# Performance work log

Hardware: AMD Instinct MI355X
Metric: run time of the kernel (lower is better)

The kernel has to match this reference:

```python
import jax, jax.numpy as jnp
import numpy as np

B, T, C, H = 4, 4096, 1024, 64

def setup_inputs() -> dict:
    key = jax.random.key(0)
    kx, kk, kq, kv = jax.random.split(key, 4)
    x = jax.random.normal(kx, (B, T, C), dtype=jnp.float32)
    # causal lower-triangular mask; masked_fill where mask == 0
    mask = jnp.tril(jnp.ones((T, T), dtype=jnp.int32))
    s = 1.0 / np.sqrt(C)
    Wk = jax.random.normal(kk, (H, C), dtype=jnp.float32) * s
    Wq = jax.random.normal(kq, (H, C), dtype=jnp.float32) * s
    Wv = jax.random.normal(kv, (H, C), dtype=jnp.float32) * s
    return {"x": x, "mask": mask, "Wk": Wk, "Wq": Wq, "Wv": Wv}

def reference(x, mask, Wk, Wq, Wv):
    # single-head attention; dropout is identity in eval mode
    scale = Wk.shape[0] ** -0.5  # head_size ** -0.5
    k = jnp.einsum('btc,hc->bth', x, Wk)  # [B,T,H]
    q = jnp.einsum('btc,hc->bth', x, Wq)
    v = jnp.einsum('btc,hc->bth', x, Wv)
    att = jnp.einsum('bqh,bkh->bqk', q, k) * scale  # [B,T,T]
    att = jnp.where(mask == 0, -jnp.inf, att)
    att = jax.nn.softmax(att, axis=-1)
    out = jnp.einsum('bqk,bkh->bqh', att, v)  # [B,T,H]
    return out
```

## Files before the change

### kernel.cpp

```cpp
#include <hip/hip_runtime.h>
#include <hip/hip_bf16.h>

#define BT 16384
#define CDIM 1024
#define HD 64
#define TT 4096

typedef __bf16 bf16x8 __attribute__((ext_vector_type(8)));
typedef __bf16 bf16x4 __attribute__((ext_vector_type(4)));
typedef float f32x4 __attribute__((ext_vector_type(4)));

__device__ __forceinline__ f32x4 mfma16(bf16x8 a, bf16x8 b, f32x4 c){
  return __builtin_amdgcn_mfma_f32_16x16x32_bf16(a, b, c, 0, 0, 0);
}

__global__ __launch_bounds__(256) void wconv_k(const float* __restrict__ Wk,
    const float* __restrict__ Wq, const float* __restrict__ Wv,
    __bf16* __restrict__ Wbf){
  int idx = blockIdx.x*256 + threadIdx.x;
  int e0 = idx*4;
  int n = e0 >> 10;
  int c = e0 & 1023;
  const float* src; float s;
  if (n < 64)      { src = Wk + (size_t)n*CDIM;       s = 1.0f;   }
  else if (n < 128){ src = Wq + (size_t)(n-64)*CDIM;  s = 0.125f; }
  else             { src = Wv + (size_t)(n-128)*CDIM; s = 1.0f;   }
  float4 v = *reinterpret_cast<const float4*>(src + c);
  __bf16* dst = Wbf + e0;
  dst[0]=(__bf16)(v.x*s); dst[1]=(__bf16)(v.y*s);
  dst[2]=(__bf16)(v.z*s); dst[3]=(__bf16)(v.w*s);
}

__global__ __launch_bounds__(512) void proj_k(const float* __restrict__ x,
    const __bf16* __restrict__ Wbf, __bf16* __restrict__ kb,
    __bf16* __restrict__ qb, __bf16* __restrict__ vTb){
  __shared__ __bf16 Wt[192][72];
  __shared__ __bf16 Xt[64][72];

  const int tid  = threadIdx.x;
  const int lane = tid & 63;
  const int w    = tid >> 6;
  const int wr   = w >> 2;
  const int wn   = w & 3;
  const int l15  = lane & 15, g = lane >> 4;
  const long row0 = (long)blockIdx.x*64;

  f32x4 acc[2][3];
  #pragma unroll
  for (int a=0;a<2;a++)
    #pragma unroll
    for (int b=0;b<3;b++) acc[a][b] = (f32x4)(0.0f);

  for (int kk=0; kk<16; ++kk){
    const int kk0 = kk*64;
    __syncthreads();
    #pragma unroll
    for (int i=0;i<3;i++){
      const int c  = tid + 512*i;
      const int rw = c >> 3, c8 = (c & 7)*8;
      bf16x8 wv = *reinterpret_cast<const bf16x8*>(Wbf + (size_t)rw*CDIM + kk0 + c8);
      *reinterpret_cast<bf16x8*>(&Wt[rw][c8]) = wv;
    }
    {
      const int rw = tid >> 3, c8 = (tid & 7)*8;
      const float* src = x + (row0 + rw)*CDIM + kk0 + c8;
      float4 lo = *reinterpret_cast<const float4*>(src);
      float4 hi = *reinterpret_cast<const float4*>(src + 4);
      bf16x8 xv;
      xv[0]=(__bf16)lo.x; xv[1]=(__bf16)lo.y; xv[2]=(__bf16)lo.z; xv[3]=(__bf16)lo.w;
      xv[4]=(__bf16)hi.x; xv[5]=(__bf16)hi.y; xv[6]=(__bf16)hi.z; xv[7]=(__bf16)hi.w;
      *reinterpret_cast<bf16x8*>(&Xt[rw][c8]) = xv;
    }
    __syncthreads();

    bf16x8 a0[2], a1[2], b0[3], b1[3];
    #pragma unroll
    for (int rf=0;rf<2;rf++){
      a0[rf] = *reinterpret_cast<const bf16x8*>(&Xt[wr*32 + rf*16 + l15][g*8]);
      a1[rf] = *reinterpret_cast<const bf16x8*>(&Xt[wr*32 + rf*16 + l15][g*8 + 32]);
    }
    #pragma unroll
    for (int nf=0;nf<3;nf++){
      b0[nf] = *reinterpret_cast<const bf16x8*>(&Wt[wn*48 + nf*16 + l15][g*8]);
      b1[nf] = *reinterpret_cast<const bf16x8*>(&Wt[wn*48 + nf*16 + l15][g*8 + 32]);
    }
    #pragma unroll
    for (int rf=0;rf<2;rf++)
      #pragma unroll
      for (int nf=0;nf<3;nf++)
        acc[rf][nf] = mfma16(a1[rf], b1[nf], mfma16(a0[rf], b0[nf], acc[rf][nf]));
  }

  const long bidx = row0 >> 12;
  #pragma unroll
  for (int nf=0;nf<3;nf++){
    const int n0  = wn*48 + nf*16 + l15;
    const int mat = n0 >> 6;
    const int h   = n0 & 63;
    #pragma unroll
    for (int rf=0;rf<2;rf++){
      const long rbase = row0 + wr*32 + rf*16 + g*4;
      if (mat == 0){
        #pragma unroll
        for (int r=0;r<4;r++) kb[(rbase+r)*HD + h] = (__bf16)acc[rf][nf][r];
      } else if (mat == 1){
        #pragma unroll
        for (int r=0;r<4;r++) qb[(rbase+r)*HD + h] = (__bf16)acc[rf][nf][r];
      } else {
        bf16x4 t4;
        #pragma unroll
        for (int r=0;r<4;r++) t4[r] = (__bf16)acc[rf][nf][r];
        *reinterpret_cast<bf16x4*>(vTb + (bidx*64 + h)*TT + (rbase & 4095)) = t4;
      }
    }
  }
}

template<int NS>
__global__ __launch_bounds__(256) void attn_part_k(const __bf16* __restrict__ kbg,
    const __bf16* __restrict__ qbg, const __bf16* __restrict__ vT,
    __bf16* __restrict__ po, float* __restrict__ pl){
  __shared__ __bf16 Klds[64][68];
  __shared__ __bf16 Vlds[64][68];
  __shared__ __bf16 Plds[4][16][68];

  const int tid  = threadIdx.x;
  const int lane = tid & 63;
  const int w    = tid >> 6;
  const int l15  = lane & 15, g = lane >> 4;

  const int bi  = blockIdx.x;
  const int b   = bi / (64*NS);
  const int rem = bi % (64*NS);
  const int qt  = 63 - rem / NS;
  const int s   = rem % NS;

  const int ntiles = qt + 1;
  const int lo = ( s      * ntiles) / NS;
  const int hi = ((s + 1) * ntiles) / NS;
  const int pidx = (b*64 + qt)*NS + s;

  if (lo == hi){
    if (l15 == 0){
      #pragma unroll
      for (int r=0;r<4;r++) pl[pidx*64 + w*16 + g*4 + r] = 0.0f;
    }
    return;
  }

  const long qbase = (long)b*TT + (long)qt*64;

  bf16x8 qf0, qf1;
  {
    const __bf16* src = qbg + (qbase + w*16 + l15)*HD + g*8;
    qf0 = *reinterpret_cast<const bf16x8*>(src);
    qf1 = *reinterpret_cast<const bf16x8*>(src + 32);
  }

  f32x4 o[4];
  #pragma unroll
  for (int ch=0; ch<4; ++ch) o[ch] = (f32x4)(0.0f);
  float lp[4] = {0.f, 0.f, 0.f, 0.f};

  const __bf16* vbase = vT + (size_t)b*64*TT;

  for (int kv=lo; kv<hi; ++kv){
    const long kvbase = (long)b*TT + (long)kv*64;
    const int  kvt    = kv*64;

    __syncthreads();
    {
      const int key = tid >> 2;
      const int d0  = (tid & 3) * 16;
      const __bf16* ks = kbg + (kvbase + key)*HD + d0;
      *reinterpret_cast<bf16x8*>(&Klds[key][d0])   = *reinterpret_cast<const bf16x8*>(ks);
      *reinterpret_cast<bf16x8*>(&Klds[key][d0+8]) = *reinterpret_cast<const bf16x8*>(ks+8);
      const int h    = tid >> 2;
      const int key0 = (tid & 3) * 16;
      const __bf16* vs = vbase + (size_t)h*TT + kvt + key0;
      *reinterpret_cast<bf16x8*>(&Vlds[h][key0])   = *reinterpret_cast<const bf16x8*>(vs);
      *reinterpret_cast<bf16x8*>(&Vlds[h][key0+8]) = *reinterpret_cast<const bf16x8*>(vs+8);
    }
    __syncthreads();

    f32x4 sv[4];
    #pragma unroll
    for (int c=0;c<4;c++){
      bf16x8 kb0 = *reinterpret_cast<const bf16x8*>(&Klds[c*16 + l15][g*8]);
      bf16x8 kb1 = *reinterpret_cast<const bf16x8*>(&Klds[c*16 + l15][g*8 + 32]);
      sv[c] = mfma16(qf0, kb0, (f32x4)(-16.0f));
      sv[c] = mfma16(qf1, kb1, sv[c]);
    }

    if (kv == qt){
      #pragma unroll
      for (int c=0;c<4;c++){
        const int key = c*16 + l15;
        #pragma unroll
        for (int r=0;r<4;r++){
          const int qr = w*16 + g*4 + r;
          if (key > qr) sv[c][r] = -1e30f;
        }
      }
    }

    #pragma unroll
    for (int c=0;c<4;c++){
      #pragma unroll
      for (int r=0;r<4;r++) sv[c][r] = __expf(sv[c][r]);
    }
    #pragma unroll
    for (int r=0;r<4;r++)
      lp[r] += (sv[0][r] + sv[1][r]) + (sv[2][r] + sv[3][r]);

    #pragma unroll
    for (int c=0;c<4;c++){
      #pragma unroll
      for (int r=0;r<4;r++) Plds[w][g*4+r][c*16 + l15] = (__bf16)sv[c][r];
    }
    asm volatile("s_waitcnt lgkmcnt(0)" ::: "memory");
    __builtin_amdgcn_sched_barrier(0);
    bf16x8 pa0 = *reinterpret_cast<const bf16x8*>(&Plds[w][l15][g*8]);
    bf16x8 pa1 = *reinterpret_cast<const bf16x8*>(&Plds[w][l15][g*8 + 32]);

    #pragma unroll
    for (int ch=0; ch<4; ++ch){
      bf16x8 vb0 = *reinterpret_cast<const bf16x8*>(&Vlds[ch*16 + l15][g*8]);
      bf16x8 vb1 = *reinterpret_cast<const bf16x8*>(&Vlds[ch*16 + l15][g*8 + 32]);
      o[ch] = mfma16(pa0, vb0, o[ch]);
      o[ch] = mfma16(pa1, vb1, o[ch]);
    }
  }

  float lr[4];
  #pragma unroll
  for (int r=0;r<4;r++){
    float v = lp[r];
    v += __shfl_xor(v, 1);
    v += __shfl_xor(v, 2);
    v += __shfl_xor(v, 4);
    v += __shfl_xor(v, 8);
    lr[r] = v;
  }
  float rl[4];
  #pragma unroll
  for (int r=0;r<4;r++) rl[r] = (lr[r] > 0.0f) ? 1.0f/lr[r] : 0.0f;

  __bf16* podst = po + (size_t)pidx*4096;
  #pragma unroll
  for (int ch=0; ch<4; ++ch){
    #pragma unroll
    for (int r=0;r<4;r++)
      podst[(w*16 + g*4 + r)*64 + ch*16 + l15] = (__bf16)(o[ch][r] * rl[r]);
  }
  if (l15 == 0){
    #pragma unroll
    for (int r=0;r<4;r++) pl[pidx*64 + w*16 + g*4 + r] = lr[r];
  }
}

template<int NS>
__global__ __launch_bounds__(256) void comb_k(const __bf16* __restrict__ po,
    const float* __restrict__ pl, float* __restrict__ out){
  const int idx   = blockIdx.x*256 + threadIdx.x;
  const int qrow  = idx >> 6;
  const int dim   = idx & 63;
  const int qtg   = qrow >> 6;
  const int rowin = qrow & 63;

  float num = 0.0f, den = 0.0f;
  #pragma unroll
  for (int s=0;s<NS;s++){
    const float l = pl[(qtg*NS + s)*64 + rowin];
    den += l;
    num += l * (float)po[(size_t)(qtg*NS + s)*4096 + rowin*64 + dim];
  }
  out[idx] = num / den;
}

extern "C" void kernel_launch(void* const* d_in, const int* in_sizes, int n_in,
                              void* d_out, int out_size, void* d_ws, size_t ws_size,
                              hipStream_t stream) {
  const float* x  = (const float*)d_in[0];
  const float* Wk = (const float*)d_in[2];
  const float* Wq = (const float*)d_in[3];
  const float* Wv = (const float*)d_in[4];
  float* out = (float*)d_out;

  char* ws = (char*)d_ws;
  __bf16* Wbf = (__bf16*)ws;
  __bf16* kb  = (__bf16*)(ws + 393216);
  __bf16* qb  = (__bf16*)(ws + 2490368);
  __bf16* vTb = (__bf16*)(ws + 4587520);
  __bf16* po  = (__bf16*)(ws + 6684672);

  wconv_k<<<192, 256, 0, stream>>>(Wk, Wq, Wv, Wbf);
  proj_k <<<256, 512, 0, stream>>>(x, Wbf, kb, qb, vTb);

  const size_t need8 = 6684672ull + (size_t)2048*4096*2 + (size_t)2048*64*4;
  if (ws_size >= need8){
    float* pl = (float*)(ws + 6684672 + (size_t)2048*4096*2);
    attn_part_k<8><<<2048, 256, 0, stream>>>(kb, qb, vTb, po, pl);
    comb_k<8>    <<<4096, 256, 0, stream>>>(po, pl, out);
  } else {
    float* pl = (float*)(ws + 6684672 + (size_t)1024*4096*2);
    attn_part_k<4><<<1024, 256, 0, stream>>>(kb, qb, vTb, po, pl);
    comb_k<4>    <<<4096, 256, 0, stream>>>(po, pl, out);
  }
}
```

Before: 65.26 us.

## Register-prefetch next tiles in projection and attention loops

Both the projection GEMM loop and the attention KV loop now load the next tile's global data into registers right after the LDS barrier, then write it to shared memory at the start of the next iteration. The aim is to hide global-memory latency behind the MFMA compute of the current tile. This adds register pressure, which could lower occupancy.

```diff
diff --git a/kernel.cpp b/kernel.cpp
--- a/kernel.cpp
+++ b/kernel.cpp
@@ -45,33 +45,50 @@
   const int l15  = lane & 15, g = lane >> 4;
   const long row0 = (long)blockIdx.x*64;
 
+  const int wrw[3] = { (tid)>>3, (tid+512)>>3, (tid+1024)>>3 };
+  const int wc8[3] = { (tid&7)*8, (tid&7)*8, (tid&7)*8 };
+  const int xrw = tid >> 3, xc8 = (tid & 7)*8;
+
   f32x4 acc[2][3];
   #pragma unroll
   for (int a=0;a<2;a++)
     #pragma unroll
     for (int b=0;b<3;b++) acc[a][b] = (f32x4)(0.0f);
 
+  bf16x8 wreg[3];
+  float4 xlo, xhi;
+
+  #pragma unroll
+  for (int i=0;i<3;i++)
+    wreg[i] = *reinterpret_cast<const bf16x8*>(Wbf + (size_t)wrw[i]*CDIM + wc8[i]);
+  {
+    const float* src = x + (row0 + xrw)*CDIM + xc8;
+    xlo = *reinterpret_cast<const float4*>(src);
+    xhi = *reinterpret_cast<const float4*>(src + 4);
+  }
+
   for (int kk=0; kk<16; ++kk){
-    const int kk0 = kk*64;
     __syncthreads();
     #pragma unroll
-    for (int i=0;i<3;i++){
-      const int c  = tid + 512*i;
-      const int rw = c >> 3, c8 = (c & 7)*8;
-      bf16x8 wv = *reinterpret_cast<const bf16x8*>(Wbf + (size_t)rw*CDIM + kk0 + c8);
-      *reinterpret_cast<bf16x8*>(&Wt[rw][c8]) = wv;
-    }
+    for (int i=0;i<3;i++)
+      *reinterpret_cast<bf16x8*>(&Wt[wrw[i]][wc8[i]]) = wreg[i];
     {
-      const int rw = tid >> 3, c8 = (tid & 7)*8;
-      const float* src = x + (row0 + rw)*CDIM + kk0 + c8;
-      float4 lo = *reinterpret_cast<const float4*>(src);
-      float4 hi = *reinterpret_cast<const float4*>(src + 4);
       bf16x8 xv;
-      xv[0]=(__bf16)lo.x; xv[1]=(__bf16)lo.y; xv[2]=(__bf16)lo.z; xv[3]=(__bf16)lo.w;
-      xv[4]=(__bf16)hi.x; xv[5]=(__bf16)hi.y; xv[6]=(__bf16)hi.z; xv[7]=(__bf16)hi.w;
-      *reinterpret_cast<bf16x8*>(&Xt[rw][c8]) = xv;
+      xv[0]=(__bf16)xlo.x; xv[1]=(__bf16)xlo.y; xv[2]=(__bf16)xlo.z; xv[3]=(__bf16)xlo.w;
+      xv[4]=(__bf16)xhi.x; xv[5]=(__bf16)xhi.y; xv[6]=(__bf16)xhi.z; xv[7]=(__bf16)xhi.w;
+      *reinterpret_cast<bf16x8*>(&Xt[xrw][xc8]) = xv;
     }
     __syncthreads();
+
+    if (kk < 15){
+      const int nk0 = (kk+1)*64;
+      #pragma unroll
+      for (int i=0;i<3;i++)
+        wreg[i] = *reinterpret_cast<const bf16x8*>(Wbf + (size_t)wrw[i]*CDIM + nk0 + wc8[i]);
+      const float* src = x + (row0 + xrw)*CDIM + nk0 + xc8;
+      xlo = *reinterpret_cast<const float4*>(src);
+      xhi = *reinterpret_cast<const float4*>(src + 4);
+    }
 
     bf16x8 a0[2], a1[2], b0[3], b1[3];
     #pragma unroll
@@ -164,24 +181,37 @@
 
   const __bf16* vbase = vT + (size_t)b*64*TT;
 
+  const int skey = tid >> 2;
+  const int sd0  = (tid & 3) * 16;
+  bf16x8 kr0, kr1, vr0, vr1;
+
+  {
+    const long kvbase = (long)b*TT + (long)lo*64;
+    const __bf16* ks = kbg + (kvbase + skey)*HD + sd0;
+    kr0 = *reinterpret_cast<const bf16x8*>(ks);
+    kr1 = *reinterpret_cast<const bf16x8*>(ks+8);
+    const __bf16* vs = vbase + (size_t)skey*TT + lo*64 + sd0;
+    vr0 = *reinterpret_cast<const bf16x8*>(vs);
+    vr1 = *reinterpret_cast<const bf16x8*>(vs+8);
+  }
+
   for (int kv=lo; kv<hi; ++kv){
-    const long kvbase = (long)b*TT + (long)kv*64;
-    const int  kvt    = kv*64;
-
     __syncthreads();
-    {
-      const int key = tid >> 2;
-      const int d0  = (tid & 3) * 16;
-      const __bf16* ks = kbg + (kvbase + key)*HD + d0;
-      *reinterpret_cast<bf16x8*>(&Klds[key][d0])   = *reinterpret_cast<const bf16x8*>(ks);
-      *reinterpret_cast<bf16x8*>(&Klds[key][d0+8]) = *reinterpret_cast<const bf16x8*>(ks+8);
-      const int h    = tid >> 2;
-      const int key0 = (tid & 3) * 16;
-      const __bf16* vs = vbase + (size_t)h*TT + kvt + key0;
-      *reinterpret_cast<bf16x8*>(&Vlds[h][key0])   = *reinterpret_cast<const bf16x8*>(vs);
-      *reinterpret_cast<bf16x8*>(&Vlds[h][key0+8]) = *reinterpret_cast<const bf16x8*>(vs+8);
-    }
+    *reinterpret_cast<bf16x8*>(&Klds[skey][sd0])   = kr0;
+    *reinterpret_cast<bf16x8*>(&Klds[skey][sd0+8]) = kr1;
+    *reinterpret_cast<bf16x8*>(&Vlds[skey][sd0])   = vr0;
+    *reinterpret_cast<bf16x8*>(&Vlds[skey][sd0+8]) = vr1;
     __syncthreads();
+
+    if (kv+1 < hi){
+      const long nbase = (long)b*TT + (long)(kv+1)*64;
+      const __bf16* ks = kbg + (nbase + skey)*HD + sd0;
+      kr0 = *reinterpret_cast<const bf16x8*>(ks);
+      kr1 = *reinterpret_cast<const bf16x8*>(ks+8);
+      const __bf16* vs = vbase + (size_t)skey*TT + (kv+1)*64 + sd0;
+      vr0 = *reinterpret_cast<const bf16x8*>(vs);
+      vr1 = *reinterpret_cast<const bf16x8*>(vs+8);
+    }
 
     f32x4 sv[4];
     #pragma unroll
```

Result: faster. 63.71 us (-2.4%).
